# Optimization experiments

Measured on AMD Instinct MI355X. Metric: run time of the kernel, lower is better.

Reference implementation:

```python
import jax, jax.numpy as jnp
import numpy as np
from jax import lax

B, FREQ, TIME = 64, 128, 400
HID, STEPS, NCLS = 256, 50, 2
EPS = 1e-5
SLOPE = 25.0  # fast_sigmoid surrogate slope

@jax.custom_vjp
def spike(x):
    return (x > 0).astype(x.dtype)

def _spike_fwd(x):
    return (x > 0).astype(x.dtype), x

def _spike_bwd(x, g):
    return (g / (SLOPE * jnp.abs(x) + 1.0) ** 2,)

spike.defvjp(_spike_fwd, _spike_bwd)

def layernorm(x, g, b):
    m = x.mean(-1, keepdims=True)
    v = ((x - m) ** 2).mean(-1, keepdims=True)
    return (x - m) * lax.rsqrt(v + EPS) * g + b

def bn_eval(x, g, b, m, v):
    # eval-mode BatchNorm2d with running stats, x: (B,C,H,W)
    sh = (1, -1, 1, 1)
    return (x - m.reshape(sh)) * lax.rsqrt(v.reshape(sh) + EPS) * g.reshape(sh) + b.reshape(sh)

def conv3x3(x, w, b):
    y = lax.conv_general_dilated(x, w, (1, 1), 'SAME',
                                 dimension_numbers=('NCHW', 'OIHW', 'NCHW'))
    return y + b.reshape(1, -1, 1, 1)

def maxpool2(x):
    return lax.reduce_window(x, -jnp.inf, lax.max, (1, 1, 2, 2), (1, 1, 2, 2), 'VALID')

def interp_linear(h, out_size):
    # F.interpolate(mode='linear', align_corners=False); h: (B,C,Tin)
    Tin = h.shape[-1]
    src = (jnp.arange(out_size, dtype=h.dtype) + 0.5) * (Tin / out_size) - 0.5
    src = jnp.clip(src, 0.0, Tin - 1)
    lo = jnp.floor(src).astype(jnp.int32)
    hi = jnp.minimum(lo + 1, Tin - 1)
    w = src - lo.astype(h.dtype)
    return h[..., lo] * (1.0 - w) + h[..., hi] * w

def lif(cur, mem, beta, thr):
    # snntorch Leaky, reset_mechanism='subtract': reset from previous mem (detached)
    b = jnp.clip(beta, 0.0, 1.0)
    reset = lax.stop_gradient((mem > thr).astype(mem.dtype))
    mem = b * mem + cur - reset * thr
    spk = spike(mem - thr)
    return spk, mem

def setup_inputs() -> dict:
    key = jax.random.key(0)
    ks = jax.random.split(key, 8)
    rn = lambda k, s, sc: jax.random.normal(k, s, jnp.float32) * sc
    f32 = lambda v: jnp.asarray(v, jnp.float32)
    return dict(
        x=rn(ks[0], (B, 1, FREQ, TIME), 1.0),
        c1w=rn(ks[1], (32, 1, 3, 3), 0.3), c1b=jnp.zeros((32,), jnp.float32),
        bn1g=jnp.ones((32,), jnp.float32), bn1b=jnp.zeros((32,), jnp.float32),
        bn1m=jnp.zeros((32,), jnp.float32), bn1v=jnp.ones((32,), jnp.float32),
        c2w=rn(ks[2], (64, 32, 3, 3), 0.06), c2b=jnp.zeros((64,), jnp.float32),
        bn2g=jnp.ones((64,), jnp.float32), bn2b=jnp.zeros((64,), jnp.float32),
        bn2m=jnp.zeros((64,), jnp.float32), bn2v=jnp.ones((64,), jnp.float32),
        pw=rn(ks[3], (64, HID), 0.125), pb=jnp.zeros((HID,), jnp.float32),
        plg=jnp.ones((HID,), jnp.float32), plb=jnp.zeros((HID,), jnp.float32),
        ing=jnp.ones((HID,), jnp.float32), inb=jnp.zeros((HID,), jnp.float32),
        fc1w=rn(ks[4], (HID, HID), 0.0625), fc1b=jnp.zeros((HID,), jnp.float32),
        fc2w=rn(ks[5], (HID, HID // 2), 0.0625), fc2b=jnp.zeros((HID // 2,), jnp.float32),
        fcow=rn(ks[6], (HID // 2, NCLS), 0.0884), fcob=jnp.zeros((NCLS,), jnp.float32),
        beta1=f32(0.8), thr1=f32(1.0),
        beta2=f32(0.8), thr2=f32(1.0),
        beta3=f32(0.8), thr3=f32(1.0),
    )

def reference(x, c1w, c1b, bn1g, bn1b, bn1m, bn1v, c2w, c2b, bn2g, bn2b, bn2m, bn2v,
              pw, pb, plg, plb, ing, inb, fc1w, fc1b, fc2w, fc2b, fcow, fcob,
              beta1, thr1, beta2, thr2, beta3, thr3):
    Bb = x.shape[0]
    # encoder
    h = maxpool2(jax.nn.relu(bn_eval(conv3x3(x, c1w, c1b), bn1g, bn1b, bn1m, bn1v)))
    h = maxpool2(jax.nn.relu(bn_eval(conv3x3(h, c2w, c2b), bn2g, bn2b, bn2m, bn2v)))
    h = h.mean(axis=2)                 # (B, 64, T/4) mean over freq
    h = h.transpose(0, 2, 1)           # (B, T/4, 64)
    h = layernorm(h @ pw + pb, plg, plb)   # channel_proj + LN -> (B, T/4, HID)
    h = h.transpose(0, 2, 1)           # (B, HID, T/4)
    h = interp_linear(h, STEPS)        # (B, HID, STEPS)
    cur = layernorm(h.transpose(0, 2, 1), ing, inb)  # (B, STEPS, HID)
    # fc1 hoisted out of the time loop (depends only on currents)
    cur1 = jnp.einsum('bth,hk->btk', cur, fc1w) + fc1b  # (B, STEPS, HID)

    def step(carry, c1):
        m1, m2, mo = carry
        s1, m1 = lif(c1, m1, beta1, thr1)
        s2, m2 = lif(s1 @ fc2w + fc2b, m2, beta2, thr2)
        _, mo = lif(s2 @ fcow + fcob, mo, beta3, thr3)
        return (m1, m2, mo), (s1, mo)

    init = (jnp.zeros((Bb, HID), x.dtype),
            jnp.zeros((Bb, HID // 2), x.dtype),
            jnp.zeros((Bb, NCLS), x.dtype))
    _, (spk_rec, mo_rec) = lax.scan(step, init, cur1.transpose(1, 0, 2))
    logits = mo_rec.sum(0)                      # (B, NCLS)
    spike_record = spk_rec.transpose(1, 0, 2)   # (B, STEPS, HID)
    return logits, spike_record
```

## Files before the change

kernel.cpp:

```cpp
#include <hip/hip_runtime.h>
#include <math.h>

#define P1H 66
#define P1W 208
#define P1PLANE (P1H * P1W)


__global__ __launch_bounds__(256) void k0_border(float* __restrict__ p1p) {
  int plane = blockIdx.x;
  float* base = p1p + (size_t)plane * P1PLANE;
  for (int i = threadIdx.x; i < 544; i += 256) {
    int r, c;
    if (i < 208)      { r = 0;            c = i; }
    else if (i < 416) { r = 65;           c = i - 208; }
    else if (i < 480) { r = i - 416 + 1;  c = 0; }
    else              { r = i - 480 + 1;  c = 201; }
    base[r * P1W + c] = 0.f;
  }
}

__global__ __launch_bounds__(256) void k1_conv1(
    const float* __restrict__ x,  const float* __restrict__ c1w,
    const float* __restrict__ c1b, const float* __restrict__ g1,
    const float* __restrict__ b1, const float* __restrict__ m1,
    const float* __restrict__ v1, float* __restrict__ p1p) {
  __shared__ float tile[18][67];
  __shared__ float scale[32], shift[32];
  int wx = blockIdx.x, hy = blockIdx.y, b = blockIdx.z;
  int tid = threadIdx.x;
  int gy0 = hy * 16 - 1, gx0 = wx * 64 - 1;
  const float* xb = x + (size_t)b * 128 * 400;
  for (int i = tid; i < 18 * 66; i += 256) {
    int r = i / 66, c = i - r * 66;
    int gr = gy0 + r, gc = gx0 + c;
    float v = 0.f;
    if (gr >= 0 && gr < 128 && gc >= 0 && gc < 400) v = xb[gr * 400 + gc];
    tile[r][c] = v;
  }
  if (tid < 32) {
    double s = (double)g1[tid] / sqrt((double)v1[tid] + 1e-5);
    scale[tid] = (float)s;
    shift[tid] = (float)(((double)c1b[tid] - (double)m1[tid]) * s + (double)b1[tid]);
  }
  __syncthreads();
  int tx = tid & 31, ty = tid >> 5;
  int pw = wx * 32 + tx;
  int ph = hy * 8 + ty;
  if (pw >= 200) return;
  float in[4][4];
#pragma unroll
  for (int r = 0; r < 4; ++r)
#pragma unroll
    for (int c = 0; c < 4; ++c) in[r][c] = tile[2 * ty + r][2 * tx + c];
  for (int ch = 0; ch < 32; ++ch) {
    float s00 = 0, s01 = 0, s10 = 0, s11 = 0;
#pragma unroll
    for (int ky = 0; ky < 3; ++ky)
#pragma unroll
      for (int kx = 0; kx < 3; ++kx) {
        float w = c1w[ch * 9 + ky * 3 + kx];
        s00 = fmaf(w, in[ky][kx],     s00);
        s01 = fmaf(w, in[ky][kx + 1], s01);
        s10 = fmaf(w, in[ky + 1][kx],     s10);
        s11 = fmaf(w, in[ky + 1][kx + 1], s11);
      }
    float sc = scale[ch], sh = shift[ch];
    float y00 = fmaxf(fmaf(sc, s00, sh), 0.f);
    float y01 = fmaxf(fmaf(sc, s01, sh), 0.f);
    float y10 = fmaxf(fmaf(sc, s10, sh), 0.f);
    float y11 = fmaxf(fmaf(sc, s11, sh), 0.f);
    float r = fmaxf(fmaxf(y00, y01), fmaxf(y10, y11));
    p1p[((size_t)(b * 32 + ch) * P1H + (ph + 1)) * P1W + (pw + 1)] = r;
  }
}

__global__ __launch_bounds__(256) void k2_conv2(
    const float* __restrict__ p1p, const float* __restrict__ c2w,
    const float* __restrict__ c2b, const float* __restrict__ g2,
    const float* __restrict__ b2, const float* __restrict__ m2,
    const float* __restrict__ v2, float* __restrict__ p2) {
  int b = blockIdx.z;
  int wid = __builtin_amdgcn_readfirstlane((int)(threadIdx.x >> 6));
  int lane = threadIdx.x & 63;
  int widx = blockIdx.x * 4 + wid;
  int ty = widx / 25, tx = widx - ty * 25;
  int ph0 = ty * 4, pw0 = tx * 4;
  const float* ipbase = p1p + (size_t)(b * 32) * P1PLANE + (ph0 * 2) * P1W + (pw0 * 2);
  float acc[8][8];
#pragma unroll
  for (int i = 0; i < 8; ++i)
#pragma unroll
    for (int j = 0; j < 8; ++j) acc[i][j] = 0.f;

  for (int ic = 0; ic < 32; ++ic) {
    float wv[9];
    const float* wp = c2w + ((lane * 32) + ic) * 9;
#pragma unroll
    for (int j = 0; j < 9; ++j) wv[j] = wp[j];
    const float* ip = ipbase + (size_t)ic * P1PLANE;
#pragma unroll
    for (int r = 0; r < 10; ++r) {
      float srow[10];
#pragma unroll
      for (int c = 0; c < 10; ++c) srow[c] = ip[r * P1W + c];
#pragma unroll
      for (int ky = 0; ky < 3; ++ky) {
        int yo = r - ky;
        if (yo >= 0 && yo <= 7) {
#pragma unroll
          for (int xo = 0; xo < 8; ++xo) {
            acc[yo][xo] = fmaf(srow[xo + 0], wv[ky * 3 + 0], acc[yo][xo]);
            acc[yo][xo] = fmaf(srow[xo + 1], wv[ky * 3 + 1], acc[yo][xo]);
            acc[yo][xo] = fmaf(srow[xo + 2], wv[ky * 3 + 2], acc[yo][xo]);
          }
        }
      }
    }
  }
  int oc = lane;
  double sd = (double)g2[oc] / sqrt((double)v2[oc] + 1e-5);
  float sc = (float)sd;
  float sh = (float)(((double)c2b[oc] - (double)m2[oc]) * sd + (double)b2[oc]);
#pragma unroll
  for (int py = 0; py < 4; ++py)
#pragma unroll
    for (int px = 0; px < 4; ++px) {
      float q00 = fmaxf(fmaf(sc, acc[2 * py][2 * px],         sh), 0.f);
      float q01 = fmaxf(fmaf(sc, acc[2 * py][2 * px + 1],     sh), 0.f);
      float q10 = fmaxf(fmaf(sc, acc[2 * py + 1][2 * px],     sh), 0.f);
      float q11 = fmaxf(fmaf(sc, acc[2 * py + 1][2 * px + 1], sh), 0.f);
      float r = fmaxf(fmaxf(q00, q01), fmaxf(q10, q11));
      p2[((size_t)(b * 64 + oc) * 32 + (ph0 + py)) * 100 + (pw0 + px)] = r;
    }
}

__global__ __launch_bounds__(256) void k3_mean(const float* __restrict__ p2,
                                               double* __restrict__ hm) {
  int idx = blockIdx.x * 256 + threadIdx.x;
  int xcol = idx % 100;
  int bc = idx / 100;
  const float* p = p2 + (size_t)bc * 3200 + xcol;
  double s = 0.0;
#pragma unroll
  for (int h = 0; h < 32; ++h) s += (double)p[h * 100];
  hm[idx] = s * (1.0 / 32.0);
}

__device__ __forceinline__ double block_reduce_sum_256(double v, double* sbuf) {
#pragma unroll
  for (int off = 32; off > 0; off >>= 1) v += __shfl_down(v, off, 64);
  int lane = threadIdx.x & 63, wid = threadIdx.x >> 6;
  __syncthreads();
  if (lane == 0) sbuf[wid] = v;
  __syncthreads();
  return sbuf[0] + sbuf[1] + sbuf[2] + sbuf[3];
}

__global__ __launch_bounds__(256) void k4_proj_ln(
    const double* __restrict__ hm, const float* __restrict__ pw,
    const float* __restrict__ pb, const float* __restrict__ plg,
    const float* __restrict__ plb, double* __restrict__ hproj) {
  __shared__ double hv[64];
  __shared__ double sbuf[4];
  int bt = blockIdx.x;
  int b = bt / 100, t = bt - b * 100;
  int k = threadIdx.x;
  if (k < 64) hv[k] = hm[(b * 64 + k) * 100 + t];
  __syncthreads();
  double s = (double)pb[k];
#pragma unroll 8
  for (int c = 0; c < 64; ++c) s = fma(hv[c], (double)pw[c * 256 + k], s);
  double mean = block_reduce_sum_256(s, sbuf) * (1.0 / 256.0);
  double d = s - mean;
  double var = block_reduce_sum_256(d * d, sbuf) * (1.0 / 256.0);
  double inv = 1.0 / sqrt(var + 1e-5);
  hproj[(size_t)bt * 256 + k] = d * inv * (double)plg[k] + (double)plb[k];
}

__global__ __launch_bounds__(256) void k5_interp_ln_fc1(
    const double* __restrict__ hproj, const float* __restrict__ ing,
    const float* __restrict__ inb, const float* __restrict__ fc1w,
    const float* __restrict__ fc1b, double* __restrict__ cur1) {
  __shared__ double curs[256];
  __shared__ double sbuf[4];
  int bs = blockIdx.x;
  int b = bs / 50, st = bs - b * 50;
  int k = threadIdx.x;
  const double* hp = hproj + (size_t)(b * 100 + 2 * st) * 256;
  double xk = 0.5 * (hp[k] + hp[256 + k]);
  double mean = block_reduce_sum_256(xk, sbuf) * (1.0 / 256.0);
  double d = xk - mean;
  double var = block_reduce_sum_256(d * d, sbuf) * (1.0 / 256.0);
  double inv = 1.0 / sqrt(var + 1e-5);
  curs[k] = d * inv * (double)ing[k] + (double)inb[k];
  __syncthreads();
  double s = (double)fc1b[k];
#pragma unroll 8
  for (int c = 0; c < 256; ++c) s = fma(curs[c], (double)fc1w[c * 256 + k], s);
  cur1[(size_t)bs * 256 + k] = s;
}

__global__ __launch_bounds__(256) void k6_lif1(
    const double* __restrict__ cur1, const float* __restrict__ beta1p,
    const float* __restrict__ thr1p, float* __restrict__ dout) {
  int b = blockIdx.x, k = threadIdx.x;
  double beta = (double)beta1p[0];
  beta = beta < 0.0 ? 0.0 : (beta > 1.0 ? 1.0 : beta);
  double thr = (double)thr1p[0];
  double mem = 0.0;
  float* srec = dout + 128;
  for (int t = 0; t < 50; ++t) {
    double c = cur1[(size_t)(b * 50 + t) * 256 + k];
    mem = beta * mem + c - ((mem > thr) ? thr : 0.0);
    srec[(size_t)(b * 50 + t) * 256 + k] = (mem > thr) ? 1.0f : 0.0f;
  }
}

__global__ __launch_bounds__(128) void k7_fc2(
    const float* __restrict__ dout, const float* __restrict__ fc2w,
    const float* __restrict__ fc2b, double* __restrict__ cur2) {
  __shared__ float s1s[256];
  int bt = blockIdx.x;
  int j = threadIdx.x;
  const float* srec = dout + 128;
  s1s[j] = srec[(size_t)bt * 256 + j];
  s1s[j + 128] = srec[(size_t)bt * 256 + j + 128];
  __syncthreads();
  double s = (double)fc2b[j];
#pragma unroll 8
  for (int c = 0; c < 256; ++c) s = fma((double)s1s[c], (double)fc2w[c * 128 + j], s);
  cur2[(size_t)bt * 128 + j] = s;
}

__global__ __launch_bounds__(128) void k8_tail(
    const double* __restrict__ cur2, const float* __restrict__ fcow,
    const float* __restrict__ fcob, const float* __restrict__ beta2p,
    const float* __restrict__ thr2p, const float* __restrict__ beta3p,
    const float* __restrict__ thr3p, float* __restrict__ dout) {
  __shared__ double red[2][2];
  int b = blockIdx.x, j = threadIdx.x;
  double beta2 = (double)beta2p[0];
  beta2 = beta2 < 0.0 ? 0.0 : (beta2 > 1.0 ? 1.0 : beta2);
  double thr2 = (double)thr2p[0];
  double beta3 = (double)beta3p[0];
  beta3 = beta3 < 0.0 ? 0.0 : (beta3 > 1.0 ? 1.0 : beta3);
  double thr3 = (double)thr3p[0];
  double fw0 = (double)fcow[j * 2 + 0], fw1 = (double)fcow[j * 2 + 1];
  double m2 = 0.0, mo0 = 0.0, mo1 = 0.0, l0 = 0.0, l1 = 0.0;
  int wid = j >> 6, lane = j & 63;
  for (int t = 0; t < 50; ++t) {
    double c2 = cur2[(size_t)(b * 50 + t) * 128 + j];
    m2 = beta2 * m2 + c2 - ((m2 > thr2) ? thr2 : 0.0);
    double s2v = (m2 > thr2) ? 1.0 : 0.0;
    double p0 = s2v * fw0, p1 = s2v * fw1;
#pragma unroll
    for (int off = 32; off > 0; off >>= 1) {
      p0 += __shfl_down(p0, off, 64);
      p1 += __shfl_down(p1, off, 64);
    }
    if (lane == 0) { red[wid][0] = p0; red[wid][1] = p1; }
    __syncthreads();
    if (j == 0) {
      double c30 = red[0][0] + red[1][0] + (double)fcob[0];
      double c31 = red[0][1] + red[1][1] + (double)fcob[1];
      mo0 = beta3 * mo0 + c30 - ((mo0 > thr3) ? thr3 : 0.0);
      mo1 = beta3 * mo1 + c31 - ((mo1 > thr3) ? thr3 : 0.0);
      l0 += mo0; l1 += mo1;
    }
    __syncthreads();
  }
  if (j == 0) { dout[b * 2 + 0] = (float)l0; dout[b * 2 + 1] = (float)l1; }
}

extern "C" void kernel_launch(void* const* d_in, const int* in_sizes, int n_in,
                              void* d_out, int out_size, void* d_ws, size_t ws_size,
                              hipStream_t stream) {
  const float* x    = (const float*)d_in[0];
  const float* c1w  = (const float*)d_in[1];
  const float* c1b  = (const float*)d_in[2];
  const float* bn1g = (const float*)d_in[3];
  const float* bn1b = (const float*)d_in[4];
  const float* bn1m = (const float*)d_in[5];
  const float* bn1v = (const float*)d_in[6];
  const float* c2w  = (const float*)d_in[7];
  const float* c2b  = (const float*)d_in[8];
  const float* bn2g = (const float*)d_in[9];
  const float* bn2b = (const float*)d_in[10];
  const float* bn2m = (const float*)d_in[11];
  const float* bn2v = (const float*)d_in[12];
  const float* pw   = (const float*)d_in[13];
  const float* pb   = (const float*)d_in[14];
  const float* plg  = (const float*)d_in[15];
  const float* plb  = (const float*)d_in[16];
  const float* ing  = (const float*)d_in[17];
  const float* inb  = (const float*)d_in[18];
  const float* fc1w = (const float*)d_in[19];
  const float* fc1b = (const float*)d_in[20];
  const float* fc2w = (const float*)d_in[21];
  const float* fc2b = (const float*)d_in[22];
  const float* fcow = (const float*)d_in[23];
  const float* fcob = (const float*)d_in[24];
  const float* beta1 = (const float*)d_in[25];
  const float* thr1  = (const float*)d_in[26];
  const float* beta2 = (const float*)d_in[27];
  const float* thr2  = (const float*)d_in[28];
  const float* beta3 = (const float*)d_in[29];
  const float* thr3  = (const float*)d_in[30];

  char* ws = (char*)d_ws;
  float*  p1p   = (float*)ws;
  float*  p2    = (float*)(ws + 112459776ULL);
  double* hm    = (double*)ws;
  double* hproj = (double*)(ws + 3276800ULL);
  double* cur1  = (double*)(ws + 16384000ULL);
  double* cur2  = (double*)(ws + 22937600ULL);
  float* dout = (float*)d_out;

  k0_border<<<dim3(2048), 256, 0, stream>>>(p1p);
  k1_conv1<<<dim3(7, 8, 64), 256, 0, stream>>>(x, c1w, c1b, bn1g, bn1b, bn1m, bn1v, p1p);
  k2_conv2<<<dim3(50, 1, 64), 256, 0, stream>>>(p1p, c2w, c2b, bn2g, bn2b, bn2m, bn2v, p2);
  k3_mean<<<dim3(1600), 256, 0, stream>>>(p2, hm);
  k4_proj_ln<<<dim3(6400), 256, 0, stream>>>(hm, pw, pb, plg, plb, hproj);
  k5_interp_ln_fc1<<<dim3(3200), 256, 0, stream>>>(hproj, ing, inb, fc1w, fc1b, cur1);
  k6_lif1<<<dim3(64), 256, 0, stream>>>(cur1, beta1, thr1, dout);
  k7_fc2<<<dim3(3200), 128, 0, stream>>>(dout, fc2w, fc2b, cur2);
  k8_tail<<<dim3(64), 128, 0, stream>>>(cur2, fcow, fcob, beta2, thr2, beta3, thr3, dout);
}
```

Before: 575.7 us.

## Retile conv2, batch rows in projection/fc GEMMs, split serial LIF tail kernels

Conv2 now gives each wave a 4x8 output tile instead of 8x8, halving accumulator registers and doubling the grid, with a launch-bounds occupancy hint. The projection, fc1 and fc2 GEMM kernels each process 4 or 8 rows per block so every weight load is reused across rows. The interp+LN step is separated from fc1. The LIF kernels are split into more, smaller blocks, and the output layer's per-step block syncs are replaced by a parallel per-timestep dot product followed by a short serial scan. This targets register pressure, redundant weight traffic and serialized syncs, at the cost of extra launches and intermediate buffers.

```diff
diff --git a/kernel.cpp b/kernel.cpp
--- a/kernel.cpp
+++ b/kernel.cpp
@@ -74,7 +74,7 @@
   }
 }
 
-__global__ __launch_bounds__(256) void k2_conv2(
+__global__ __launch_bounds__(256, 6) void k2_conv2(
     const float* __restrict__ p1p, const float* __restrict__ c2w,
     const float* __restrict__ c2b, const float* __restrict__ g2,
     const float* __restrict__ b2, const float* __restrict__ m2,
@@ -84,11 +84,11 @@
   int lane = threadIdx.x & 63;
   int widx = blockIdx.x * 4 + wid;
   int ty = widx / 25, tx = widx - ty * 25;
-  int ph0 = ty * 4, pw0 = tx * 4;
-  const float* ipbase = p1p + (size_t)(b * 32) * P1PLANE + (ph0 * 2) * P1W + (pw0 * 2);
-  float acc[8][8];
-#pragma unroll
-  for (int i = 0; i < 8; ++i)
+  int r0 = ty * 4, c0 = tx * 8;
+  const float* ipbase = p1p + (size_t)(b * 32) * P1PLANE + r0 * P1W + c0;
+  float acc[4][8];
+#pragma unroll
+  for (int i = 0; i < 4; ++i)
 #pragma unroll
     for (int j = 0; j < 8; ++j) acc[i][j] = 0.f;
 
@@ -99,19 +99,19 @@
     for (int j = 0; j < 9; ++j) wv[j] = wp[j];
     const float* ip = ipbase + (size_t)ic * P1PLANE;
 #pragma unroll
-    for (int r = 0; r < 10; ++r) {
+    for (int l = 0; l < 6; ++l) {
       float srow[10];
 #pragma unroll
-      for (int c = 0; c < 10; ++c) srow[c] = ip[r * P1W + c];
-#pragma unroll
-      for (int ky = 0; ky < 3; ++ky) {
-        int yo = r - ky;
-        if (yo >= 0 && yo <= 7) {
+      for (int c = 0; c < 10; ++c) srow[c] = ip[l * P1W + c];
+#pragma unroll
+      for (int o = 0; o < 4; ++o) {
+        int ky = l - o;
+        if (ky >= 0 && ky <= 2) {
 #pragma unroll
           for (int xo = 0; xo < 8; ++xo) {
-            acc[yo][xo] = fmaf(srow[xo + 0], wv[ky * 3 + 0], acc[yo][xo]);
-            acc[yo][xo] = fmaf(srow[xo + 1], wv[ky * 3 + 1], acc[yo][xo]);
-            acc[yo][xo] = fmaf(srow[xo + 2], wv[ky * 3 + 2], acc[yo][xo]);
+            acc[o][xo] = fmaf(srow[xo + 0], wv[ky * 3 + 0], acc[o][xo]);
+            acc[o][xo] = fmaf(srow[xo + 1], wv[ky * 3 + 1], acc[o][xo]);
+            acc[o][xo] = fmaf(srow[xo + 2], wv[ky * 3 + 2], acc[o][xo]);
           }
         }
       }
@@ -122,7 +122,7 @@
   float sc = (float)sd;
   float sh = (float)(((double)c2b[oc] - (double)m2[oc]) * sd + (double)b2[oc]);
 #pragma unroll
-  for (int py = 0; py < 4; ++py)
+  for (int py = 0; py < 2; ++py)
 #pragma unroll
     for (int px = 0; px < 4; ++px) {
       float q00 = fmaxf(fmaf(sc, acc[2 * py][2 * px],         sh), 0.f);
@@ -130,7 +130,7 @@
       float q10 = fmaxf(fmaf(sc, acc[2 * py + 1][2 * px],     sh), 0.f);
       float q11 = fmaxf(fmaf(sc, acc[2 * py + 1][2 * px + 1], sh), 0.f);
       float r = fmaxf(fmaxf(q00, q01), fmaxf(q10, q11));
-      p2[((size_t)(b * 64 + oc) * 32 + (ph0 + py)) * 100 + (pw0 + px)] = r;
+      p2[((size_t)(b * 64 + oc) * 32 + (ty * 2 + py)) * 100 + (tx * 4 + px)] = r;
     }
 }
 
@@ -160,28 +160,38 @@
     const double* __restrict__ hm, const float* __restrict__ pw,
     const float* __restrict__ pb, const float* __restrict__ plg,
     const float* __restrict__ plb, double* __restrict__ hproj) {
-  __shared__ double hv[64];
   __shared__ double sbuf[4];
-  int bt = blockIdx.x;
-  int b = bt / 100, t = bt - b * 100;
+  int bt0 = blockIdx.x * 4;
+  int b = bt0 / 100, t0 = bt0 - b * 100;
   int k = threadIdx.x;
-  if (k < 64) hv[k] = hm[(b * 64 + k) * 100 + t];
-  __syncthreads();
-  double s = (double)pb[k];
-#pragma unroll 8
-  for (int c = 0; c < 64; ++c) s = fma(hv[c], (double)pw[c * 256 + k], s);
-  double mean = block_reduce_sum_256(s, sbuf) * (1.0 / 256.0);
-  double d = s - mean;
-  double var = block_reduce_sum_256(d * d, sbuf) * (1.0 / 256.0);
-  double inv = 1.0 / sqrt(var + 1e-5);
-  hproj[(size_t)bt * 256 + k] = d * inv * (double)plg[k] + (double)plb[k];
-}
-
-__global__ __launch_bounds__(256) void k5_interp_ln_fc1(
+  double accv[4];
+  double pbk = (double)pb[k];
+#pragma unroll
+  for (int r = 0; r < 4; ++r) accv[r] = pbk;
+  const double* hmb = hm + (size_t)b * 64 * 100 + t0;
+#pragma unroll 4
+  for (int c = 0; c < 64; ++c) {
+    double w = (double)pw[c * 256 + k];
+    const double* hp = hmb + c * 100;
+    accv[0] = fma(hp[0], w, accv[0]);
+    accv[1] = fma(hp[1], w, accv[1]);
+    accv[2] = fma(hp[2], w, accv[2]);
+    accv[3] = fma(hp[3], w, accv[3]);
+  }
+  double gk = (double)plg[k], bk = (double)plb[k];
+#pragma unroll
+  for (int r = 0; r < 4; ++r) {
+    double mean = block_reduce_sum_256(accv[r], sbuf) * (1.0 / 256.0);
+    double d = accv[r] - mean;
+    double var = block_reduce_sum_256(d * d, sbuf) * (1.0 / 256.0);
+    double inv = 1.0 / sqrt(var + 1e-5);
+    hproj[(size_t)(bt0 + r) * 256 + k] = d * inv * gk + bk;
+  }
+}
+
+__global__ __launch_bounds__(256) void k5a_interp_ln(
     const double* __restrict__ hproj, const float* __restrict__ ing,
-    const float* __restrict__ inb, const float* __restrict__ fc1w,
-    const float* __restrict__ fc1b, double* __restrict__ cur1) {
-  __shared__ double curs[256];
+    const float* __restrict__ inb, double* __restrict__ curs) {
   __shared__ double sbuf[4];
   int bs = blockIdx.x;
   int b = bs / 50, st = bs - b * 50;
@@ -192,18 +202,35 @@
   double d = xk - mean;
   double var = block_reduce_sum_256(d * d, sbuf) * (1.0 / 256.0);
   double inv = 1.0 / sqrt(var + 1e-5);
-  curs[k] = d * inv * (double)ing[k] + (double)inb[k];
-  __syncthreads();
-  double s = (double)fc1b[k];
-#pragma unroll 8
-  for (int c = 0; c < 256; ++c) s = fma(curs[c], (double)fc1w[c * 256 + k], s);
-  cur1[(size_t)bs * 256 + k] = s;
-}
-
-__global__ __launch_bounds__(256) void k6_lif1(
+  curs[(size_t)bs * 256 + k] = d * inv * (double)ing[k] + (double)inb[k];
+}
+
+__global__ __launch_bounds__(256) void k5b_fc1(
+    const double* __restrict__ curs, const float* __restrict__ fc1w,
+    const float* __restrict__ fc1b, double* __restrict__ cur1) {
+  int row0 = blockIdx.x * 8;
+  int k = threadIdx.x;
+  double accv[8];
+  double bk = (double)fc1b[k];
+#pragma unroll
+  for (int r = 0; r < 8; ++r) accv[r] = bk;
+  const double* ab = curs + (size_t)row0 * 256;
+#pragma unroll 4
+  for (int c = 0; c < 256; ++c) {
+    double w = (double)fc1w[c * 256 + k];
+#pragma unroll
+    for (int r = 0; r < 8; ++r)
+      accv[r] = fma(ab[(size_t)r * 256 + c], w, accv[r]);
+  }
+#pragma unroll
+  for (int r = 0; r < 8; ++r) cur1[(size_t)(row0 + r) * 256 + k] = accv[r];
+}
+
+__global__ __launch_bounds__(64) void k6_lif1(
     const double* __restrict__ cur1, const float* __restrict__ beta1p,
     const float* __restrict__ thr1p, float* __restrict__ dout) {
-  int b = blockIdx.x, k = threadIdx.x;
+  int b = blockIdx.x >> 2;
+  int k = ((blockIdx.x & 3) << 6) + threadIdx.x;
   double beta = (double)beta1p[0];
   beta = beta < 0.0 ? 0.0 : (beta > 1.0 ? 1.0 : beta);
   double thr = (double)thr1p[0];
@@ -219,57 +246,70 @@
 __global__ __launch_bounds__(128) void k7_fc2(
     const float* __restrict__ dout, const float* __restrict__ fc2w,
     const float* __restrict__ fc2b, double* __restrict__ cur2) {
-  __shared__ float s1s[256];
-  int bt = blockIdx.x;
+  int row0 = blockIdx.x * 8;
   int j = threadIdx.x;
   const float* srec = dout + 128;
-  s1s[j] = srec[(size_t)bt * 256 + j];
-  s1s[j + 128] = srec[(size_t)bt * 256 + j + 128];
-  __syncthreads();
-  double s = (double)fc2b[j];
-#pragma unroll 8
-  for (int c = 0; c < 256; ++c) s = fma((double)s1s[c], (double)fc2w[c * 128 + j], s);
-  cur2[(size_t)bt * 128 + j] = s;
-}
-
-__global__ __launch_bounds__(128) void k8_tail(
-    const double* __restrict__ cur2, const float* __restrict__ fcow,
-    const float* __restrict__ fcob, const float* __restrict__ beta2p,
-    const float* __restrict__ thr2p, const float* __restrict__ beta3p,
-    const float* __restrict__ thr3p, float* __restrict__ dout) {
-  __shared__ double red[2][2];
-  int b = blockIdx.x, j = threadIdx.x;
+  double accv[8];
+  double bj = (double)fc2b[j];
+#pragma unroll
+  for (int r = 0; r < 8; ++r) accv[r] = bj;
+#pragma unroll 4
+  for (int c = 0; c < 256; ++c) {
+    double w = (double)fc2w[c * 128 + j];
+#pragma unroll
+    for (int r = 0; r < 8; ++r)
+      accv[r] = fma((double)srec[(size_t)(row0 + r) * 256 + c], w, accv[r]);
+  }
+#pragma unroll
+  for (int r = 0; r < 8; ++r) cur2[(size_t)(row0 + r) * 128 + j] = accv[r];
+}
+
+__global__ __launch_bounds__(64) void k8a_lif2(
+    const double* __restrict__ cur2, const float* __restrict__ beta2p,
+    const float* __restrict__ thr2p, float* __restrict__ s2f) {
+  int idx = blockIdx.x * 64 + threadIdx.x;
+  int b = idx >> 7, j = idx & 127;
   double beta2 = (double)beta2p[0];
   beta2 = beta2 < 0.0 ? 0.0 : (beta2 > 1.0 ? 1.0 : beta2);
   double thr2 = (double)thr2p[0];
-  double beta3 = (double)beta3p[0];
-  beta3 = beta3 < 0.0 ? 0.0 : (beta3 > 1.0 ? 1.0 : beta3);
-  double thr3 = (double)thr3p[0];
-  double fw0 = (double)fcow[j * 2 + 0], fw1 = (double)fcow[j * 2 + 1];
-  double m2 = 0.0, mo0 = 0.0, mo1 = 0.0, l0 = 0.0, l1 = 0.0;
-  int wid = j >> 6, lane = j & 63;
+  double m2 = 0.0;
   for (int t = 0; t < 50; ++t) {
     double c2 = cur2[(size_t)(b * 50 + t) * 128 + j];
     m2 = beta2 * m2 + c2 - ((m2 > thr2) ? thr2 : 0.0);
-    double s2v = (m2 > thr2) ? 1.0 : 0.0;
-    double p0 = s2v * fw0, p1 = s2v * fw1;
-#pragma unroll
-    for (int off = 32; off > 0; off >>= 1) {
-      p0 += __shfl_down(p0, off, 64);
-      p1 += __shfl_down(p1, off, 64);
+    s2f[(size_t)(b * 50 + t) * 128 + j] = (m2 > thr2) ? 1.0f : 0.0f;
+  }
+}
+
+__global__ __launch_bounds__(64) void k8b_out(
+    const float* __restrict__ s2f, const float* __restrict__ fcow,
+    const float* __restrict__ fcob, const float* __restrict__ beta3p,
+    const float* __restrict__ thr3p, float* __restrict__ dout) {
+  __shared__ double c3s[50][2];
+  int b = blockIdx.x, t = threadIdx.x;
+  if (t < 50) {
+    double c30 = (double)fcob[0], c31 = (double)fcob[1];
+    const float* sp = s2f + (size_t)(b * 50 + t) * 128;
+#pragma unroll 4
+    for (int jj = 0; jj < 128; ++jj) {
+      double s = (double)sp[jj];
+      c30 = fma(s, (double)fcow[jj * 2 + 0], c30);
+      c31 = fma(s, (double)fcow[jj * 2 + 1], c31);
     }
-    if (lane == 0) { red[wid][0] = p0; red[wid][1] = p1; }
-    __syncthreads();
-    if (j == 0) {
-      double c30 = red[0][0] + red[1][0] + (double)fcob[0];
-      double c31 = red[0][1] + red[1][1] + (double)fcob[1];
-      mo0 = beta3 * mo0 + c30 - ((mo0 > thr3) ? thr3 : 0.0);
-      mo1 = beta3 * mo1 + c31 - ((mo1 > thr3) ? thr3 : 0.0);
+    c3s[t][0] = c30; c3s[t][1] = c31;
+  }
+  __syncthreads();
+  if (t == 0) {
+    double beta3 = (double)beta3p[0];
+    beta3 = beta3 < 0.0 ? 0.0 : (beta3 > 1.0 ? 1.0 : beta3);
+    double thr3 = (double)thr3p[0];
+    double mo0 = 0.0, mo1 = 0.0, l0 = 0.0, l1 = 0.0;
+    for (int tt = 0; tt < 50; ++tt) {
+      mo0 = beta3 * mo0 + c3s[tt][0] - ((mo0 > thr3) ? thr3 : 0.0);
+      mo1 = beta3 * mo1 + c3s[tt][1] - ((mo1 > thr3) ? thr3 : 0.0);
       l0 += mo0; l1 += mo1;
     }
-    __syncthreads();
-  }
-  if (j == 0) { dout[b * 2 + 0] = (float)l0; dout[b * 2 + 1] = (float)l1; }
+    dout[b * 2 + 0] = (float)l0; dout[b * 2 + 1] = (float)l1;
+  }
 }
 
 extern "C" void kernel_launch(void* const* d_in, const int* in_sizes, int n_in,
@@ -312,17 +352,21 @@
   float*  p2    = (float*)(ws + 112459776ULL);
   double* hm    = (double*)ws;
   double* hproj = (double*)(ws + 3276800ULL);
-  double* cur1  = (double*)(ws + 16384000ULL);
-  double* cur2  = (double*)(ws + 22937600ULL);
+  double* curs  = (double*)(ws + 16384000ULL);
+  double* cur1  = (double*)(ws + 22937600ULL);
+  double* cur2  = (double*)(ws + 29491200ULL);
+  float*  s2f   = (float*)(ws + 32768000ULL);
   float* dout = (float*)d_out;
 
   k0_border<<<dim3(2048), 256, 0, stream>>>(p1p);
   k1_conv1<<<dim3(7, 8, 64), 256, 0, stream>>>(x, c1w, c1b, bn1g, bn1b, bn1m, bn1v, p1p);
-  k2_conv2<<<dim3(50, 1, 64), 256, 0, stream>>>(p1p, c2w, c2b, bn2g, bn2b, bn2m, bn2v, p2);
+  k2_conv2<<<dim3(100, 1, 64), 256, 0, stream>>>(p1p, c2w, c2b, bn2g, bn2b, bn2m, bn2v, p2);
   k3_mean<<<dim3(1600), 256, 0, stream>>>(p2, hm);
-  k4_proj_ln<<<dim3(6400), 256, 0, stream>>>(hm, pw, pb, plg, plb, hproj);
-  k5_interp_ln_fc1<<<dim3(3200), 256, 0, stream>>>(hproj, ing, inb, fc1w, fc1b, cur1);
-  k6_lif1<<<dim3(64), 256, 0, stream>>>(cur1, beta1, thr1, dout);
-  k7_fc2<<<dim3(3200), 128, 0, stream>>>(dout, fc2w, fc2b, cur2);
-  k8_tail<<<dim3(64), 128, 0, stream>>>(cur2, fcow, fcob, beta2, thr2, beta3, thr3, dout);
-}
+  k4_proj_ln<<<dim3(1600), 256, 0, stream>>>(hm, pw, pb, plg, plb, hproj);
+  k5a_interp_ln<<<dim3(3200), 256, 0, stream>>>(hproj, ing, inb, curs);
+  k5b_fc1<<<dim3(400), 256, 0, stream>>>(curs, fc1w, fc1b, cur1);
+  k6_lif1<<<dim3(256), 64, 0, stream>>>(cur1, beta1, thr1, dout);
+  k7_fc2<<<dim3(400), 128, 0, stream>>>(dout, fc2w, fc2b, cur2);
+  k8a_lif2<<<dim3(128), 64, 0, stream>>>(cur2, beta2, thr2, s2f);
+  k8b_out<<<dim3(64), 64, 0, stream>>>(s2f, fcow, fcob, beta3, thr3, dout);
+}
```

New measurement: 584.7 us. About the same (+1.6%).
